# Performance work log

Measured on AMD Instinct MI355X. Metric: run time of the kernel, lower is better.

## Reference

```python
import jax, jax.numpy as jnp
import numpy as np

B, T, C, H, HS = 2, 2048, 1024, 16, 64
W_SIZE = 128
BLK = 64
NB = T // BLK            # 32 blocks
NSEL = 8                 # selected blocks per (b, h)
EPS = 1e-8


def setup_inputs() -> dict:
    key = jax.random.key(0)
    ks = jax.random.split(key, 12)
    s = 0.02
    return {
        "hidden_states": jax.random.normal(ks[0], (B, T, C), dtype=jnp.float32),
        "Wq": jax.random.normal(ks[1], (C, C), dtype=jnp.float32) * s,
        "bq": jnp.zeros((C,), jnp.float32),
        "Wk": jax.random.normal(ks[2], (C, C), dtype=jnp.float32) * s,
        "bk": jnp.zeros((C,), jnp.float32),
        "Wv": jax.random.normal(ks[3], (C, C), dtype=jnp.float32) * s,
        "bv": jnp.zeros((C,), jnp.float32),
        "Wo": jax.random.normal(ks[4], (C, C), dtype=jnp.float32) * s,
        "bo": jnp.zeros((C,), jnp.float32),
        "Wg": jax.random.normal(ks[5], (C, 3), dtype=jnp.float32) * s,
        "bg": jnp.zeros((3,), jnp.float32),
    }


def _sdpa(q, k, v, mask):
    # q: [B,H,Tq,HS], k/v: [B,H,S,HS], mask: [Tq,S] bool (True = attend)
    scale = 1.0 / jnp.sqrt(jnp.asarray(HS, q.dtype))
    scores = jnp.einsum('bhqd,bhkd->bhqk', q, k) * scale
    scores = jnp.where(mask, scores, jnp.asarray(-jnp.inf, scores.dtype))
    return jnp.einsum('bhqk,bhkd->bhqd', jax.nn.softmax(scores, axis=-1), v)


def _forward(x, Wq, bq, Wk, bk, Wv, bv, Wo, bo, Wg, bg):
    q = (x @ Wq + bq).reshape(B, T, H, HS).transpose(0, 2, 1, 3)
    k = (x @ Wk + bk).reshape(B, T, H, HS).transpose(0, 2, 1, 3)
    v = (x @ Wv + bv).reshape(B, T, H, HS).transpose(0, 2, 1, 3)

    gates = jax.nn.softmax(x @ Wg + bg, axis=-1)  # [B,T,3]
    g_sl, g_sel, g_cmp = gates[..., 0:1], gates[..., 1:2], gates[..., 2:3]

    i = jnp.arange(T)[:, None]

    # --- sliding-window branch (causal AND within window band) ---
    j = jnp.arange(T)[None, :]
    slide_mask = (j <= i) & (i - j <= W_SIZE)
    out_sl = _sdpa(q, k, v, slide_mask)

    # --- block representatives (mean-pooled K/V blocks) ---
    kb = k.reshape(B, H, NB, BLK, HS)
    vb = v.reshape(B, H, NB, BLK, HS)
    k_rep = kb.mean(axis=3)  # [B,H,NB,HS]

    # cosine similarity of each query vs each block rep, averaged over T
    qn = q / jnp.maximum(jnp.linalg.norm(q, axis=-1, keepdims=True), EPS)
    kn = k_rep / jnp.maximum(jnp.linalg.norm(k_rep, axis=-1, keepdims=True), EPS)
    global_scores = jnp.einsum('bhtd,bhnd->bhtn', qn, kn).mean(axis=2)  # [B,H,NB]
    _, top_idx = jax.lax.top_k(global_scores, NSEL)  # [B,H,NSEL]

    # gather selected K/V blocks
    sel_k = jnp.take_along_axis(kb, top_idx[..., None, None], axis=2).reshape(B, H, NSEL * BLK, HS)
    sel_v = jnp.take_along_axis(vb, top_idx[..., None, None], axis=2).reshape(B, H, NSEL * BLK, HS)

    # torch is_causal with Tq != S is top-left aligned: allow j <= i
    js = jnp.arange(NSEL * BLK)[None, :]
    out_sel = _sdpa(q, sel_k, sel_v, js <= i)

    # --- compressed branch over block reps ---
    v_cmp = vb.mean(axis=3)  # [B,H,NB,HS]
    jc = jnp.arange(NB)[None, :]
    out_cmp = _sdpa(q, k_rep, v_cmp, jc <= i)

    def merge(o):
        return o.transpose(0, 2, 1, 3).reshape(B, T, C)

    out = g_sl * merge(out_sl) + g_sel * merge(out_sel) + g_cmp * merge(out_cmp)
    return out @ Wo + bo


def reference(hidden_states, Wq, bq, Wk, bk, Wv, bv, Wo, bo, Wg, bg):
    return _forward(hidden_states, Wq, bq, Wk, bk, Wv, bv, Wo, bo, Wg, bg)
```

## Files before the change

kernel.cpp:

```cpp
#include <hip/hip_runtime.h>
#include <hip/hip_bf16.h>
#include <math.h>

#define Bc   2
#define Tc   2048
#define Cc   1024
#define Hc   16
#define HSc  64
#define WSZ  128
#define BLKc 64
#define NBc  32
#define NSELc 8
#define Mrows (Bc*Tc)
#define QCH  32
#define SOFT_C 4.0f

typedef __attribute__((ext_vector_type(8))) _Float16 half8;
typedef __attribute__((ext_vector_type(4))) float f32x4v;
typedef __attribute__((ext_vector_type(8))) unsigned short ushort8v;

__device__ __forceinline__ float wave_sum(float v) {
    #pragma unroll
    for (int o = 32; o; o >>= 1) v += __shfl_xor(v, o);
    return v;
}

__device__ __forceinline__ unsigned short f2h(float f) {
    _Float16 h = (_Float16)f;
    unsigned short u;
    __builtin_memcpy(&u, &h, 2);
    return u;
}
__device__ __forceinline__ float h2f(unsigned short u) {
    _Float16 h;
    __builtin_memcpy(&h, &u, 2);
    return (float)h;
}

__device__ __forceinline__ void gload16(const void* g, void* l) {
    __builtin_amdgcn_global_load_lds(
        (const __attribute__((address_space(1))) void*)g,
        (__attribute__((address_space(3))) void*)l, 16, 0, 0);
}

__global__ __launch_bounds__(256)
void cvt_gates_kernel(const float* __restrict__ x, unsigned short* __restrict__ xb,
                      const float* __restrict__ Wg, const float* __restrict__ bg,
                      float* __restrict__ gates)
{
    if (blockIdx.x < 4096) {
        int i = (blockIdx.x * 256 + threadIdx.x) * 4;
        float4 v = *(const float4*)&x[i];
        ushort4 o;
        o.x = f2h(v.x); o.y = f2h(v.y); o.z = f2h(v.z); o.w = f2h(v.w);
        *(ushort4*)&xb[i] = o;
        return;
    }
    const int row  = (blockIdx.x - 4096) * 4 + (threadIdx.x >> 6);
    const int lane = threadIdx.x & 63;
    const float* xr = x + (size_t)row * Cc;
    float p0 = 0, p1 = 0, p2 = 0;
    #pragma unroll
    for (int it = 0; it < 4; ++it) {
        int k4 = lane * 4 + it * 256;
        float4 xv = *(const float4*)&xr[k4];
        float4 w0 = *(const float4*)&Wg[k4 * 3];
        float4 w1 = *(const float4*)&Wg[k4 * 3 + 4];
        float4 w2 = *(const float4*)&Wg[k4 * 3 + 8];
        p0 += xv.x * w0.x + xv.y * w0.w + xv.z * w1.z + xv.w * w2.y;
        p1 += xv.x * w0.y + xv.y * w1.x + xv.z * w1.w + xv.w * w2.z;
        p2 += xv.x * w0.z + xv.y * w1.y + xv.z * w2.x + xv.w * w2.w;
    }
    p0 = wave_sum(p0); p1 = wave_sum(p1); p2 = wave_sum(p2);
    if (lane == 0) {
        p0 += bg[0]; p1 += bg[1]; p2 += bg[2];
        float m = fmaxf(p0, fmaxf(p1, p2));
        float e0 = expf(p0 - m), e1 = expf(p1 - m), e2 = expf(p2 - m);
        float s = e0 + e1 + e2;
        gates[row * 3 + 0] = e0 / s;
        gates[row * 3 + 1] = e1 / s;
        gates[row * 3 + 2] = e2 / s;
    }
}

__global__ __launch_bounds__(256)
void cvt_wT4_kernel(const float* __restrict__ W0, const float* __restrict__ W1,
                    const float* __restrict__ W2, const float* __restrict__ W3,
                    unsigned short* __restrict__ D012, unsigned short* __restrict__ D3)
{
    __shared__ float tile[64][65];
    const int z = blockIdx.z;
    const float* W = (z == 0) ? W0 : (z == 1) ? W1 : (z == 2) ? W2 : W3;
    unsigned short* WT = (z < 3) ? (D012 + (size_t)z * 1024 * 1024) : D3;
    const int n0 = blockIdx.x * 64, k0 = blockIdx.y * 64;
    const int tid = threadIdx.x;
    #pragma unroll
    for (int it = 0; it < 16; ++it) {
        int lin = tid + it * 256;
        int r = lin >> 6, c = lin & 63;
        tile[r][c] = W[(size_t)(k0 + r) * 1024 + n0 + c];
    }
    __syncthreads();
    #pragma unroll
    for (int it = 0; it < 16; ++it) {
        int lin = tid + it * 256;
        int n = lin >> 6, k = lin & 63;
        WT[(size_t)(n0 + n) * 1024 + k0 + k] = f2h(tile[k][n]);
    }
}


#define FENCE asm volatile("" ::: "memory")
#define BAR() do { FENCE; __builtin_amdgcn_s_barrier(); FENCE; } while(0)
#define WAIT_LGKM0() do { asm volatile("s_waitcnt lgkmcnt(0)" ::: "memory"); \
                          __builtin_amdgcn_sched_barrier(0); } while(0)
#define WAIT_VM(N) do { asm volatile("s_waitcnt vmcnt(" #N ")" ::: "memory"); } while(0)

#define LDA(BUF, MH) do { \
    const unsigned short* _p = &lds[BUF][0][(wmo + (MH)*64 + r16) * 64]; \
    a0[0] = *(const half8*)(_p +        cc0); a1[0] = *(const half8*)(_p +        cc1); \
    a0[1] = *(const half8*)(_p + 1024 + cc0); a1[1] = *(const half8*)(_p + 1024 + cc1); \
    a0[2] = *(const half8*)(_p + 2048 + cc0); a1[2] = *(const half8*)(_p + 2048 + cc1); \
    a0[3] = *(const half8*)(_p + 3072 + cc0); a1[3] = *(const half8*)(_p + 3072 + cc1); \
} while(0)

#define LDB(BUF, NH) do { \
    const unsigned short* _p = &lds[BUF][1][(wno + (NH)*32 + r16) * 64]; \
    b0[0] = *(const half8*)(_p +        cc0); b1[0] = *(const half8*)(_p +        cc1); \
    b0[1] = *(const half8*)(_p + 1024 + cc0); b1[1] = *(const half8*)(_p + 1024 + cc1); \
} while(0)

#define CLP(I, J, MH, NH) \
    acc[(MH)*4+(I)][(NH)*2+(J)] = __builtin_amdgcn_mfma_f32_16x16x32_f16(a0[I], b0[J], acc[(MH)*4+(I)][(NH)*2+(J)], 0, 0, 0); \
    acc[(MH)*4+(I)][(NH)*2+(J)] = __builtin_amdgcn_mfma_f32_16x16x32_f16(a1[I], b1[J], acc[(MH)*4+(I)][(NH)*2+(J)], 0, 0, 0);
#define CL(MH, NH) do { \
    __builtin_amdgcn_s_setprio(1); \
    CLP(0,0,MH,NH) CLP(0,1,MH,NH) CLP(1,0,MH,NH) CLP(1,1,MH,NH) \
    CLP(2,0,MH,NH) CLP(2,1,MH,NH) CLP(3,0,MH,NH) CLP(3,1,MH,NH) \
    __builtin_amdgcn_s_setprio(0); \
} while(0)

#define STAGEA(BUF, G, TILE) do { \
    size_t _co = (size_t)(TILE) * 64 + scol_x; \
    gload16(Ag + (size_t)(m0 +       (G)*64 + wid*8 + l8) * 1024 + _co, \
            &lds[BUF][0][((G)*64 + wid*8) * 64]); \
    gload16(Ag + (size_t)(m0 + 128 + (G)*64 + wid*8 + l8) * 1024 + _co, \
            &lds[BUF][0][(128 + (G)*64 + wid*8) * 64]); \
} while(0)

#define STAGEB(BUF, G, TILE) do { \
    size_t _co = (size_t)(TILE) * 64 + scol_x; \
    int _r0 = (wid >> 2) * 64 + (G)*32 + (wid & 3) * 8; \
    gload16(BTg + (size_t)(n0 +       _r0 + l8) * 1024 + _co, \
            &lds[BUF][1][_r0 * 64]); \
    gload16(BTg + (size_t)(n0 + 128 + _r0 + l8) * 1024 + _co, \
            &lds[BUF][1][(128 + _r0) * 64]); \
} while(0)

__global__ __launch_bounds__(512, 2)
// ... 241 lines not shown
        {
            const unsigned short* qr = qbase + (size_t)lane * HSc;
            float ss = 0.f;
            #pragma unroll
            for (int d8 = 0; d8 < 8; ++d8) {
                ushort8v v8 = *(const ushort8v*)&qr[d8 * 8];
                #pragma unroll
                for (int j = 0; j < 8; ++j) { float f = h2f(v8[j]); ss += f * f; }
            }
            rinv[lane] = 1.0f / fmaxf(sqrtf(ss), 1e-8f);
        }
        float acc = 0.f;
        #pragma unroll 8
        for (int t = 0; t < 64; ++t)
            acc += h2f(qbase[(size_t)t * HSc + lane]) * rinv[t];
        qpart[((size_t)bh * QCH + nb) * HSc + lane] = acc;
    }
}

__global__ __launch_bounds__(64)
void topk_kernel(const float* __restrict__ qpart, const float* __restrict__ krep,
                 int* __restrict__ topidx)
{
    int bh = blockIdx.x, lane = threadIdx.x;
    __shared__ float sc[NBc];
    __shared__ float qbs[HSc];
    float qa = 0.0f;
    #pragma unroll
    for (int c = 0; c < QCH; c++)
        qa += qpart[((size_t)bh * QCH + c) * HSc + lane];
    qbs[lane] = qa * (1.0f / Tc);
    __syncthreads();
    if (lane < NBc) {
        float dot = 0, nk = 0;
        for (int d = 0; d < HSc; d++) {
            float kv = krep[((size_t)bh * NBc + lane) * HSc + d];
            nk += kv * kv;
            dot += qbs[d] * kv;
        }
        sc[lane] = dot / fmaxf(sqrtf(nk), 1e-8f);
    }
    __syncthreads();
    if (lane == 0) {
        for (int s = 0; s < NSELc; s++) {
            int best = 0; float bv = sc[0];
            for (int n = 1; n < NBc; n++)
                if (sc[n] > bv) { bv = sc[n]; best = n; }
            topidx[bh * NSELc + s] = best;
            sc[best] = -INFINITY;
        }
    }
}

__device__ __forceinline__ void attn_tile4(
    int p0, int wlim, int klim, int qg0, bool nomask,
    const unsigned short* __restrict__ Kh, const unsigned short* __restrict__ Vt,
    unsigned short* __restrict__ Ph,
    half8 aq0, half8 aq1, half8 ones, int wq, int l16, int quad,
    int kc0, int kc1,
    f32x4v o[4], f32x4v& o5)
{
    f32x4v s[4];
    #pragma unroll
    for (int t = 0; t < 4; ++t) {
        f32x4v sa = (f32x4v){0.f, 0.f, 0.f, 0.f};
        half8 b0 = *(const half8*)&Kh[(t * 16 + l16) * 64 + kc0];
        half8 b1 = *(const half8*)&Kh[(t * 16 + l16) * 64 + kc1];
        sa = __builtin_amdgcn_mfma_f32_16x16x32_f16(aq0, b0, sa, 0, 0, 0);
        sa = __builtin_amdgcn_mfma_f32_16x16x32_f16(aq1, b1, sa, 0, 0, 0);
        s[t] = sa;
    }

    const int prow = wq + quad * 4;
    if (nomask) {
        #pragma unroll
        for (int t = 0; t < 4; ++t) {
            int c = t * 16 + l16;
            #pragma unroll
            for (int r = 0; r < 4; ++r) {
                float p = __expf(s[t][r] - SOFT_C);
                Ph[(prow + r) * 64 + (c ^ (((prow + r) & 7) * 8))] = f2h(p);
            }
        }
    } else {
        #pragma unroll
        for (int t = 0; t < 4; ++t) {
            int kk = t * 16 + l16;
            bool kok = kk < klim;
            int jt = p0 + kk;
            #pragma unroll
            for (int r = 0; r < 4; ++r) {
                int q = qg0 + r;
                bool valid = kok && (jt <= q) && (q - jt <= wlim);
                float p = valid ? __expf(s[t][r] - SOFT_C) : 0.0f;
                Ph[(prow + r) * 64 + (kk ^ (((prow + r) & 7) * 8))] = f2h(p);
            }
        }
    }


    const int prd = (wq + l16) * 64;
    half8 ap0 = *(const half8*)&Ph[prd + kc0];
    half8 ap1 = *(const half8*)&Ph[prd + kc1];
    o5 = __builtin_amdgcn_mfma_f32_16x16x32_f16(ap0, ones, o5, 0, 0, 0);
    o5 = __builtin_amdgcn_mfma_f32_16x16x32_f16(ap1, ones, o5, 0, 0, 0);
    #pragma unroll
    for (int dt = 0; dt < 4; ++dt) {
        half8 v0 = *(const half8*)&Vt[(dt * 16 + l16) * 64 + kc0];
        half8 v1 = *(const half8*)&Vt[(dt * 16 + l16) * 64 + kc1];
        o[dt] = __builtin_amdgcn_mfma_f32_16x16x32_f16(ap0, v0, o[dt], 0, 0, 0);
        o[dt] = __builtin_amdgcn_mfma_f32_16x16x32_f16(ap1, v1, o[dt], 0, 0, 0);
    }
}

__global__ __launch_bounds__(256, 4)
void fattn_kernel(const unsigned short* __restrict__ Qh16,
                  const unsigned short* __restrict__ Kf,
                  const unsigned short* __restrict__ Vtg,
                  const unsigned short* __restrict__ krep16,
                  const unsigned short* __restrict__ vcmpT16,
                  const int* __restrict__ topidx,
                  const float* __restrict__ gates, unsigned short* __restrict__ merged)
{
    __shared__ unsigned short KH[2][64 * 64];
    __shared__ unsigned short VT[2][64 * 64];
    __shared__ unsigned short Ph[64 * 64];

    const int qt = blockIdx.x;
    const int bh = blockIdx.y;
    const int b  = bh >> 4, h = bh & 15;
    const int tid  = threadIdx.x;
    const int wid  = tid >> 6, lane = tid & 63;
    const int l16  = lane & 15, quad = lane >> 4;
    const int q0 = qt * 64;
    const int wq = wid * 16;
    const int qg0 = q0 + wq + quad * 4;

    const int nslide = (qt < 2 ? qt : 2) + 1;
    const int nsel   = (qt + 1 < NSELc) ? (qt + 1) : NSELc;
    const int nt     = nslide + nsel + 1;

    half8 aq0, aq1, ones;
    {
        const unsigned short* qrow = Qh16 + ((size_t)bh * Tc + q0 + wq + l16) * HSc;
        aq0 = *(const half8*)(qrow + quad * 8);
        aq1 = *(const half8*)(qrow + 32 + quad * 8);
        #pragma unroll
        for (int j = 0; j < 8; ++j) ones[j] = (_Float16)1.0f;
    }

    f32x4v o[4], macc[4];
    f32x4v o5 = (f32x4v){0.f, 0.f, 0.f, 0.f};
    #pragma unroll
    for (int dt = 0; dt < 4; ++dt) {
        o[dt]    = (f32x4v){0.f, 0.f, 0.f, 0.f};
        macc[dt] = (f32x4v){0.f, 0.f, 0.f, 0.f};
    }

    const int seg = tid & 7, r0 = tid >> 3;
    const int stc = (seg ^ (r0 & 7)) * 8;
    const int st0 = r0 * 64 + stc;
    const int st1 = (r0 + 32) * 64 + stc;
    const int psw = (l16 & 7) * 8;
    const int kc0 = (quad * 8) ^ psw;
    const int kc1 = (32 + quad * 8) ^ psw;

    const unsigned short* kbh = Kf  + (size_t)bh * Tc * HSc;
    const unsigned short* vbh = Vtg + (size_t)bh * HSc * Tc;

    {
        int tb0 = q0 - (nslide - 1) * 64;
        const unsigned short* kp = kbh + (size_t)tb0 * HSc;
        const unsigned short* vp = vbh + tb0;
        *(ushort8v*)&KH[0][st0] = *(const ushort8v*)(kp + (size_t)r0 * HSc + seg * 8);
        *(ushort8v*)&KH[0][st1] = *(const ushort8v*)(kp + (size_t)(r0 + 32) * HSc + seg * 8);
        *(ushort8v*)&VT[0][st0] = *(const ushort8v*)(vp + (size_t)r0 * Tc + seg * 8);
        *(ushort8v*)&VT[0][st1] = *(const ushort8v*)(vp + (size_t)(r0 + 32) * Tc + seg * 8);
    }
    __syncthreads();

    int pb = 0;
    for (int i = 0; i < nt; ++i) {
        const int cb = i & 1;
        const bool pf = (i + 1 < nt);
        ushort8v k0, k1, v0, v1;
        if (pf) {
            const int i2 = i + 1;
            int kb2, bid2;
            if (i2 < nslide)            { kb2 = q0 - (nslide - 1 - i2) * 64; bid2 = 0; }
            else if (i2 < nslide + nsel){ kb2 = topidx[bh * NSELc + (i2 - nslide)] * BLKc; bid2 = 1; }
            else                        { kb2 = 0; bid2 = 2; }
            const unsigned short *kp, *vp;
            int vs;
            if (bid2 < 2) { kp = kbh + (size_t)kb2 * HSc; vp = vbh + kb2; vs = Tc; }
            else          { kp = krep16 + (size_t)bh * 4096;
                            vp = vcmpT16 + (size_t)bh * 4096; vs = 64; }
            k0 = *(const ushort8v*)(kp + (size_t)r0 * HSc + seg * 8);
            k1 = *(const ushort8v*)(kp + (size_t)(r0 + 32) * HSc + seg * 8);
            v0 = *(const ushort8v*)(vp + (size_t)r0 * vs + seg * 8);
            v1 = *(const ushort8v*)(vp + (size_t)(r0 + 32) * vs + seg * 8);
        }

        int p0v, wl, kl, bid; bool nomask;
        if (i < nslide)            { int tb = q0 - (nslide - 1 - i) * 64;
                                     p0v = tb; wl = WSZ; kl = 64; bid = 0;
                                     nomask = (tb == q0 - 64); }
        else if (i < nslide + nsel){ int s = i - nslide;
                                     p0v = s * BLKc; wl = 1 << 30; kl = 64; bid = 1;
                                     nomask = (p0v + 63 < q0); }
        else                       { p0v = 0; wl = 1 << 30; kl = NBc; bid = 2;
                                     nomask = false; }

        if (bid != pb) {
            #pragma unroll
            for (int r = 0; r < 4; ++r) {
                float g = gates[((size_t)b * Tc + qg0 + r) * 3 + pb];
                float inv = g / o5[r];
                #pragma unroll
                for (int dt = 0; dt < 4; ++dt) { macc[dt][r] += inv * o[dt][r]; o[dt][r] = 0.f; }
                o5[r] = 0.f;
            }
            pb = bid;
        }

        attn_tile4(p0v, wl, kl, qg0, nomask, KH[cb], VT[cb], Ph,
                   aq0, aq1, ones, wq, l16, quad, kc0, kc1, o, o5);

        if (pf) {
            *(ushort8v*)&KH[cb ^ 1][st0] = k0;
            *(ushort8v*)&KH[cb ^ 1][st1] = k1;
            *(ushort8v*)&VT[cb ^ 1][st0] = v0;
            *(ushort8v*)&VT[cb ^ 1][st1] = v1;
        }
        __syncthreads();
    }
    #pragma unroll
    for (int r = 0; r < 4; ++r) {
        float g = gates[((size_t)b * Tc + qg0 + r) * 3 + 2];
        float inv = g / o5[r];
        #pragma unroll
        for (int dt = 0; dt < 4; ++dt) macc[dt][r] += inv * o[dt][r];
    }

    #pragma unroll
    for (int r = 0; r < 4; ++r) {
        size_t mrow = (size_t)b * Tc + qg0 + r;
        #pragma unroll
        for (int dt = 0; dt < 4; ++dt)
            merged[mrow * Cc + h * HSc + dt * 16 + l16] = f2h(macc[dt][r]);
    }
}

extern "C" void kernel_launch(void* const* d_in, const int* in_sizes, int n_in,
                              void* d_out, int out_size, void* d_ws, size_t ws_size,
                              hipStream_t stream)
{
    const float* x  = (const float*)d_in[0];
    const float* Wq = (const float*)d_in[1];
    const float* bq = (const float*)d_in[2];
    const float* Wk = (const float*)d_in[3];
    const float* bk = (const float*)d_in[4];
    const float* Wv = (const float*)d_in[5];
    const float* bv = (const float*)d_in[6];
    const float* Wo = (const float*)d_in[7];
    const float* bo = (const float*)d_in[8];
    const float* Wg = (const float*)d_in[9];
    const float* bg = (const float*)d_in[10];
    float* out = (float*)d_out;
    float* ws  = (float*)d_ws;

    unsigned short* Qh16 = (unsigned short*)(ws + 0);
    unsigned short* Kf16 = (unsigned short*)(ws + 2097152);
    unsigned short* Vf16 = (unsigned short*)(ws + 4194304);
    unsigned short* Vt16 = (unsigned short*)(ws + 6291456);
    unsigned short* Mgb  = (unsigned short*)(ws + 8388608);
    unsigned short* xb   = (unsigned short*)(ws + 10485760);
    unsigned short* WqkvT = (unsigned short*)(ws + 12582912);
    unsigned short* WoT   = (unsigned short*)(ws + 14155776);
    float* gates = ws + 14680064;
    float* krep  = ws + 14692352;
    unsigned short* krep16  = (unsigned short*)(ws + 14757888);
    unsigned short* vcmpT16 = (unsigned short*)(ws + 14823424);
    float* qpart = ws + 14888960;
    int*   topidx = (int*)(ws + 14954496);

    cvt_gates_kernel<<<4096 + Mrows / 4, 256, 0, stream>>>(x, xb, Wg, bg, gates);
    cvt_wT4_kernel<<<dim3(16, 16, 4), 256, 0, stream>>>(Wq, Wk, Wv, Wo, WqkvT, WoT);

    mfma_gemm_qkv8<<<dim3(12, 16), 512, 0, stream>>>(xb, WqkvT, bq, bk, bv,
                                                     Qh16, Kf16, Vf16);
    vtrans_stats_kernel<<<dim3(NBc, Bc * Hc), 256, 0, stream>>>(Kf16, Vf16, Qh16,
                                                                Vt16, krep, krep16,
                                                                vcmpT16, qpart);
    topk_kernel<<<Bc * Hc, 64, 0, stream>>>(qpart, krep, topidx);
    fattn_kernel<<<dim3(Tc / 64, Bc * Hc), 256, 0, stream>>>(Qh16, Kf16, Vt16,
                                                             krep16, vcmpT16,
                                                             topidx, gates, Mgb);
    mfma_gemm_oproj<<<dim3(8, 64), 256, 0, stream>>>(Mgb, WoT, bo, out);
}
```

Before: 199.2 us.

## Merge front conversion kernels and give each attention wave two query groups

The gate/convert kernel and the weight-transpose kernel become one launch with a linearised block index, which saves a kernel launch. The flash-attention kernel drops from 4 to 2 waves per block, and each wave now handles 32 query rows as two 16-row groups. K and V fragments loaded from LDS are reused across both groups, and each thread stages four rows instead of two. This halves LDS fragment reads per query but doubles per-wave register use and cuts the threads available to hide latency.

```diff
diff --git a/kernel.cpp b/kernel.cpp
--- a/kernel.cpp
+++ b/kernel.cpp
@@ -44,67 +44,68 @@
 }
 
 __global__ __launch_bounds__(256)
-void cvt_gates_kernel(const float* __restrict__ x, unsigned short* __restrict__ xb,
+void cvt_front_kernel(const float* __restrict__ x, unsigned short* __restrict__ xb,
                       const float* __restrict__ Wg, const float* __restrict__ bg,
-                      float* __restrict__ gates)
+                      float* __restrict__ gates,
+                      const float* __restrict__ W0, const float* __restrict__ W1,
+                      const float* __restrict__ W2, const float* __restrict__ W3,
+                      unsigned short* __restrict__ D012, unsigned short* __restrict__ D3)
 {
-    if (blockIdx.x < 4096) {
-        int i = (blockIdx.x * 256 + threadIdx.x) * 4;
+    __shared__ float tile[64][65];
+    const int bx = blockIdx.x;
+    if (bx < 4096) {
+        int i = (bx * 256 + threadIdx.x) * 4;
         float4 v = *(const float4*)&x[i];
         ushort4 o;
         o.x = f2h(v.x); o.y = f2h(v.y); o.z = f2h(v.z); o.w = f2h(v.w);
         *(ushort4*)&xb[i] = o;
         return;
     }
-    const int row  = (blockIdx.x - 4096) * 4 + (threadIdx.x >> 6);
-    const int lane = threadIdx.x & 63;
-    const float* xr = x + (size_t)row * Cc;
-    float p0 = 0, p1 = 0, p2 = 0;
-    #pragma unroll
-    for (int it = 0; it < 4; ++it) {
-        int k4 = lane * 4 + it * 256;
-        float4 xv = *(const float4*)&xr[k4];
-        float4 w0 = *(const float4*)&Wg[k4 * 3];
-        float4 w1 = *(const float4*)&Wg[k4 * 3 + 4];
-        float4 w2 = *(const float4*)&Wg[k4 * 3 + 8];
-        p0 += xv.x * w0.x + xv.y * w0.w + xv.z * w1.z + xv.w * w2.y;
-        p1 += xv.x * w0.y + xv.y * w1.x + xv.z * w1.w + xv.w * w2.z;
-        p2 += xv.x * w0.z + xv.y * w1.y + xv.z * w2.x + xv.w * w2.w;
-    }
-    p0 = wave_sum(p0); p1 = wave_sum(p1); p2 = wave_sum(p2);
-    if (lane == 0) {
-        p0 += bg[0]; p1 += bg[1]; p2 += bg[2];
-        float m = fmaxf(p0, fmaxf(p1, p2));
-        float e0 = expf(p0 - m), e1 = expf(p1 - m), e2 = expf(p2 - m);
-        float s = e0 + e1 + e2;
-        gates[row * 3 + 0] = e0 / s;
-        gates[row * 3 + 1] = e1 / s;
-        gates[row * 3 + 2] = e2 / s;
-    }
-}
-
-__global__ __launch_bounds__(256)
-void cvt_wT4_kernel(const float* __restrict__ W0, const float* __restrict__ W1,
-                    const float* __restrict__ W2, const float* __restrict__ W3,
-                    unsigned short* __restrict__ D012, unsigned short* __restrict__ D3)
-{
-    __shared__ float tile[64][65];
-    const int z = blockIdx.z;
+    if (bx < 5120) {
+        const int row  = (bx - 4096) * 4 + (threadIdx.x >> 6);
+        const int lane = threadIdx.x & 63;
+        const float* xr = x + (size_t)row * Cc;
+        float p0 = 0, p1 = 0, p2 = 0;
+        #pragma unroll
+        for (int it = 0; it < 4; ++it) {
+            int k4 = lane * 4 + it * 256;
+            float4 xv = *(const float4*)&xr[k4];
+            float4 w0 = *(const float4*)&Wg[k4 * 3];
+            float4 w1 = *(const float4*)&Wg[k4 * 3 + 4];
+            float4 w2 = *(const float4*)&Wg[k4 * 3 + 8];
+            p0 += xv.x * w0.x + xv.y * w0.w + xv.z * w1.z + xv.w * w2.y;
+            p1 += xv.x * w0.y + xv.y * w1.x + xv.z * w1.w + xv.w * w2.z;
+            p2 += xv.x * w0.z + xv.y * w1.y + xv.z * w2.x + xv.w * w2.w;
+        }
+        p0 = wave_sum(p0); p1 = wave_sum(p1); p2 = wave_sum(p2);
+        if (lane == 0) {
+            p0 += bg[0]; p1 += bg[1]; p2 += bg[2];
+            float m = fmaxf(p0, fmaxf(p1, p2));
+            float e0 = expf(p0 - m), e1 = expf(p1 - m), e2 = expf(p2 - m);
+            float s = e0 + e1 + e2;
+            gates[row * 3 + 0] = e0 / s;
+            gates[row * 3 + 1] = e1 / s;
+            gates[row * 3 + 2] = e2 / s;
+        }
+        return;
+    }
+    const int lin = bx - 5120;
+    const int z = lin >> 8;
+    const int n0 = (lin & 15) * 64, k0 = ((lin >> 4) & 15) * 64;
     const float* W = (z == 0) ? W0 : (z == 1) ? W1 : (z == 2) ? W2 : W3;
     unsigned short* WT = (z < 3) ? (D012 + (size_t)z * 1024 * 1024) : D3;
-    const int n0 = blockIdx.x * 64, k0 = blockIdx.y * 64;
     const int tid = threadIdx.x;
     #pragma unroll
     for (int it = 0; it < 16; ++it) {
-        int lin = tid + it * 256;
-        int r = lin >> 6, c = lin & 63;
+        int l2 = tid + it * 256;
+        int r = l2 >> 6, c = l2 & 63;
         tile[r][c] = W[(size_t)(k0 + r) * 1024 + n0 + c];
     }
     __syncthreads();
     #pragma unroll
     for (int it = 0; it < 16; ++it) {
-        int lin = tid + it * 256;
-        int n = lin >> 6, k = lin & 63;
+        int l2 = tid + it * 256;
+        int n = l2 >> 6, k = l2 & 63;
         WT[(size_t)(n0 + n) * 1024 + k0 + k] = f2h(tile[k][n]);
     }
 }
@@ -452,68 +453,7 @@
     }
 }
 
-__device__ __forceinline__ void attn_tile4(
-    int p0, int wlim, int klim, int qg0, bool nomask,
-    const unsigned short* __restrict__ Kh, const unsigned short* __restrict__ Vt,
-    unsigned short* __restrict__ Ph,
-    half8 aq0, half8 aq1, half8 ones, int wq, int l16, int quad,
-    int kc0, int kc1,
-    f32x4v o[4], f32x4v& o5)
-{
-    f32x4v s[4];
-    #pragma unroll
-    for (int t = 0; t < 4; ++t) {
-        f32x4v sa = (f32x4v){0.f, 0.f, 0.f, 0.f};
-        half8 b0 = *(const half8*)&Kh[(t * 16 + l16) * 64 + kc0];
-        half8 b1 = *(const half8*)&Kh[(t * 16 + l16) * 64 + kc1];
-        sa = __builtin_amdgcn_mfma_f32_16x16x32_f16(aq0, b0, sa, 0, 0, 0);
-        sa = __builtin_amdgcn_mfma_f32_16x16x32_f16(aq1, b1, sa, 0, 0, 0);
-        s[t] = sa;
-    }
-
-    const int prow = wq + quad * 4;
-    if (nomask) {
-        #pragma unroll
-        for (int t = 0; t < 4; ++t) {
-            int c = t * 16 + l16;
-            #pragma unroll
-            for (int r = 0; r < 4; ++r) {
-                float p = __expf(s[t][r] - SOFT_C);
-                Ph[(prow + r) * 64 + (c ^ (((prow + r) & 7) * 8))] = f2h(p);
-            }
-        }
-    } else {
-        #pragma unroll
-        for (int t = 0; t < 4; ++t) {
-            int kk = t * 16 + l16;
-            bool kok = kk < klim;
-            int jt = p0 + kk;
-            #pragma unroll
-            for (int r = 0; r < 4; ++r) {
-                int q = qg0 + r;
-                bool valid = kok && (jt <= q) && (q - jt <= wlim);
-                float p = valid ? __expf(s[t][r] - SOFT_C) : 0.0f;
-                Ph[(prow + r) * 64 + (kk ^ (((prow + r) & 7) * 8))] = f2h(p);
-            }
-        }
-    }
-
-
-    const int prd = (wq + l16) * 64;
-    half8 ap0 = *(const half8*)&Ph[prd + kc0];
-    half8 ap1 = *(const half8*)&Ph[prd + kc1];
-    o5 = __builtin_amdgcn_mfma_f32_16x16x32_f16(ap0, ones, o5, 0, 0, 0);
-    o5 = __builtin_amdgcn_mfma_f32_16x16x32_f16(ap1, ones, o5, 0, 0, 0);
-    #pragma unroll
-    for (int dt = 0; dt < 4; ++dt) {
-        half8 v0 = *(const half8*)&Vt[(dt * 16 + l16) * 64 + kc0];
-        half8 v1 = *(const half8*)&Vt[(dt * 16 + l16) * 64 + kc1];
-        o[dt] = __builtin_amdgcn_mfma_f32_16x16x32_f16(ap0, v0, o[dt], 0, 0, 0);
-        o[dt] = __builtin_amdgcn_mfma_f32_16x16x32_f16(ap1, v1, o[dt], 0, 0, 0);
-    }
-}
-
-__global__ __launch_bounds__(256, 4)
+__global__ __launch_bounds__(128, 2)
 void fattn_kernel(const unsigned short* __restrict__ Qh16,
                   const unsigned short* __restrict__ Kf,
                   const unsigned short* __restrict__ Vtg,
@@ -533,34 +473,41 @@
     const int wid  = tid >> 6, lane = tid & 63;
     const int l16  = lane & 15, quad = lane >> 4;
     const int q0 = qt * 64;
-    const int wq = wid * 16;
-    const int qg0 = q0 + wq + quad * 4;
+    const int wq = wid * 32;
+    const int qb0 = q0 + wq + quad * 4;
+    const int qb1 = qb0 + 16;
 
     const int nslide = (qt < 2 ? qt : 2) + 1;
     const int nsel   = (qt + 1 < NSELc) ? (qt + 1) : NSELc;
     const int nt     = nslide + nsel + 1;
 
-    half8 aq0, aq1, ones;
-    {
-        const unsigned short* qrow = Qh16 + ((size_t)bh * Tc + q0 + wq + l16) * HSc;
-        aq0 = *(const half8*)(qrow + quad * 8);
-        aq1 = *(const half8*)(qrow + 32 + quad * 8);
-        #pragma unroll
-        for (int j = 0; j < 8; ++j) ones[j] = (_Float16)1.0f;
-    }
-
-    f32x4v o[4], macc[4];
-    f32x4v o5 = (f32x4v){0.f, 0.f, 0.f, 0.f};
-    #pragma unroll
-    for (int dt = 0; dt < 4; ++dt) {
-        o[dt]    = (f32x4v){0.f, 0.f, 0.f, 0.f};
-        macc[dt] = (f32x4v){0.f, 0.f, 0.f, 0.f};
+    half8 aq[2][2], ones;
+    #pragma unroll
+    for (int qg = 0; qg < 2; ++qg) {
+        const unsigned short* qrow = Qh16 + ((size_t)bh * Tc + q0 + wq + qg * 16 + l16) * HSc;
+        aq[qg][0] = *(const half8*)(qrow + quad * 8);
+        aq[qg][1] = *(const half8*)(qrow + 32 + quad * 8);
+    }
+    #pragma unroll
+    for (int j = 0; j < 8; ++j) ones[j] = (_Float16)1.0f;
+
+    f32x4v o[2][4], macc[2][4], o5[2];
+    #pragma unroll
+    for (int qg = 0; qg < 2; ++qg) {
+        o5[qg] = (f32x4v){0.f, 0.f, 0.f, 0.f};
+        #pragma unroll
+        for (int dt = 0; dt < 4; ++dt) {
+            o[qg][dt]    = (f32x4v){0.f, 0.f, 0.f, 0.f};
+            macc[qg][dt] = (f32x4v){0.f, 0.f, 0.f, 0.f};
+        }
     }
 
     const int seg = tid & 7, r0 = tid >> 3;
     const int stc = (seg ^ (r0 & 7)) * 8;
     const int st0 = r0 * 64 + stc;
-    const int st1 = (r0 + 32) * 64 + stc;
+    const int st1 = (r0 + 16) * 64 + stc;
+    const int st2 = (r0 + 32) * 64 + stc;
+    const int st3 = (r0 + 48) * 64 + stc;
     const int psw = (l16 & 7) * 8;
     const int kc0 = (quad * 8) ^ psw;
     const int kc1 = (32 + quad * 8) ^ psw;
@@ -572,10 +519,14 @@
         int tb0 = q0 - (nslide - 1) * 64;
         const unsigned short* kp = kbh + (size_t)tb0 * HSc;
         const unsigned short* vp = vbh + tb0;
-        *(ushort8v*)&KH[0][st0] = *(const ushort8v*)(kp + (size_t)r0 * HSc + seg * 8);
-        *(ushort8v*)&KH[0][st1] = *(const ushort8v*)(kp + (size_t)(r0 + 32) * HSc + seg * 8);
-        *(ushort8v*)&VT[0][st0] = *(const ushort8v*)(vp + (size_t)r0 * Tc + seg * 8);
-        *(ushort8v*)&VT[0][st1] = *(const ushort8v*)(vp + (size_t)(r0 + 32) * Tc + seg * 8);
+        *(ushort8v*)&KH[0][st0] = *(const ushort8v*)(kp + (size_t)(r0     ) * HSc + seg * 8);
+        *(ushort8v*)&KH[0][st1] = *(const ushort8v*)(kp + (size_t)(r0 + 16) * HSc + seg * 8);
+        *(ushort8v*)&KH[0][st2] = *(const ushort8v*)(kp + (size_t)(r0 + 32) * HSc + seg * 8);
+        *(ushort8v*)&KH[0][st3] = *(const ushort8v*)(kp + (size_t)(r0 + 48) * HSc + seg * 8);
+        *(ushort8v*)&VT[0][st0] = *(const ushort8v*)(vp + (size_t)(r0     ) * Tc + seg * 8);
+        *(ushort8v*)&VT[0][st1] = *(const ushort8v*)(vp + (size_t)(r0 + 16) * Tc + seg * 8);
+        *(ushort8v*)&VT[0][st2] = *(const ushort8v*)(vp + (size_t)(r0 + 32) * Tc + seg * 8);
+        *(ushort8v*)&VT[0][st3] = *(const ushort8v*)(vp + (size_t)(r0 + 48) * Tc + seg * 8);
     }
     __syncthreads();
 
@@ -583,7 +534,7 @@
     for (int i = 0; i < nt; ++i) {
         const int cb = i & 1;
         const bool pf = (i + 1 < nt);
-        ushort8v k0, k1, v0, v1;
+        ushort8v k0, k1, k2, k3, v0, v1, v2, v3;
         if (pf) {
             const int i2 = i + 1;
             int kb2, bid2;
@@ -595,10 +546,14 @@
             if (bid2 < 2) { kp = kbh + (size_t)kb2 * HSc; vp = vbh + kb2; vs = Tc; }
             else          { kp = krep16 + (size_t)bh * 4096;
                             vp = vcmpT16 + (size_t)bh * 4096; vs = 64; }
-            k0 = *(const ushort8v*)(kp + (size_t)r0 * HSc + seg * 8);
-            k1 = *(const ushort8v*)(kp + (size_t)(r0 + 32) * HSc + seg * 8);
-            v0 = *(const ushort8v*)(vp + (size_t)r0 * vs + seg * 8);
-            v1 = *(const ushort8v*)(vp + (size_t)(r0 + 32) * vs + seg * 8);
+            k0 = *(const ushort8v*)(kp + (size_t)(r0     ) * HSc + seg * 8);
+            k1 = *(const ushort8v*)(kp + (size_t)(r0 + 16) * HSc + seg * 8);
+            k2 = *(const ushort8v*)(kp + (size_t)(r0 + 32) * HSc + seg * 8);
+            k3 = *(const ushort8v*)(kp + (size_t)(r0 + 48) * HSc + seg * 8);
+            v0 = *(const ushort8v*)(vp + (size_t)(r0     ) * vs + seg * 8);
+            v1 = *(const ushort8v*)(vp + (size_t)(r0 + 16) * vs + seg * 8);
+            v2 = *(const ushort8v*)(vp + (size_t)(r0 + 32) * vs + seg * 8);
+            v3 = *(const ushort8v*)(vp + (size_t)(r0 + 48) * vs + seg * 8);
         }
 
         int p0v, wl, kl, bid; bool nomask;
@@ -613,41 +568,127 @@
 
         if (bid != pb) {
             #pragma unroll
-            for (int r = 0; r < 4; ++r) {
-                float g = gates[((size_t)b * Tc + qg0 + r) * 3 + pb];
-                float inv = g / o5[r];
+            for (int qg = 0; qg < 2; ++qg) {
+                int qb = (qg == 0) ? qb0 : qb1;
                 #pragma unroll
-                for (int dt = 0; dt < 4; ++dt) { macc[dt][r] += inv * o[dt][r]; o[dt][r] = 0.f; }
-                o5[r] = 0.f;
+                for (int r = 0; r < 4; ++r) {
+                    float g = gates[((size_t)b * Tc + qb + r) * 3 + pb];
+                    float inv = g / o5[qg][r];
+                    #pragma unroll
+                    for (int dt = 0; dt < 4; ++dt) { macc[qg][dt][r] += inv * o[qg][dt][r]; o[qg][dt][r] = 0.f; }
+                    o5[qg][r] = 0.f;
+                }
             }
             pb = bid;
         }
 
-        attn_tile4(p0v, wl, kl, qg0, nomask, KH[cb], VT[cb], Ph,
-                   aq0, aq1, ones, wq, l16, quad, kc0, kc1, o, o5);
+        {
+            const unsigned short* Kh = KH[cb];
+            const unsigned short* Vt = VT[cb];
+            half8 bk0[4], bk1[4];
+            #pragma unroll
+            for (int t = 0; t < 4; ++t) {
+                bk0[t] = *(const half8*)&Kh[(t * 16 + l16) * 64 + kc0];
+                bk1[t] = *(const half8*)&Kh[(t * 16 + l16) * 64 + kc1];
+            }
+            f32x4v s[2][4];
+            #pragma unroll
+            for (int qg = 0; qg < 2; ++qg)
+                #pragma unroll
+                for (int t = 0; t < 4; ++t) {
+                    f32x4v sa = (f32x4v){0.f, 0.f, 0.f, 0.f};
+                    sa = __builtin_amdgcn_mfma_f32_16x16x32_f16(aq[qg][0], bk0[t], sa, 0, 0, 0);
+                    sa = __builtin_amdgcn_mfma_f32_16x16x32_f16(aq[qg][1], bk1[t], sa, 0, 0, 0);
+                    s[qg][t] = sa;
+                }
+
+            #pragma unroll
+            for (int qg = 0; qg < 2; ++qg) {
+                const int prow = wq + qg * 16 + quad * 4;
+                const int qb = (qg == 0) ? qb0 : qb1;
+                if (nomask) {
+                    #pragma unroll
+                    for (int t = 0; t < 4; ++t) {
+                        int c = t * 16 + l16;
+                        #pragma unroll
+                        for (int r = 0; r < 4; ++r) {
+                            float p = __expf(s[qg][t][r] - SOFT_C);
+                            Ph[(prow + r) * 64 + (c ^ (((prow + r) & 7) * 8))] = f2h(p);
+                        }
+                    }
+                } else {
+                    #pragma unroll
+                    for (int t = 0; t < 4; ++t) {
+                        int kk = t * 16 + l16;
+                        bool kok = kk < kl;
+                        int jt = p0v + kk;
+                        #pragma unroll
+                        for (int r = 0; r < 4; ++r) {
+                            int q = qb + r;
+                            bool valid = kok && (jt <= q) && (q - jt <= wl);
+                            float p = valid ? __expf(s[qg][t][r] - SOFT_C) : 0.0f;
+                            Ph[(prow + r) * 64 + (kk ^ (((prow + r) & 7) * 8))] = f2h(p);
+                        }
+                    }
+                }
+            }
+
+
+            half8 vv0[4], vv1[4];
+            #pragma unroll
+            for (int dt = 0; dt < 4; ++dt) {
+                vv0[dt] = *(const half8*)&Vt[(dt * 16 + l16) * 64 + kc0];
+                vv1[dt] = *(const half8*)&Vt[(dt * 16 + l16) * 64 + kc1];
+            }
+            #pragma unroll
+            for (int qg = 0; qg < 2; ++qg) {
+                const int prd = (wq + qg * 16 + l16) * 64;
+                half8 ap0 = *(const half8*)&Ph[prd + kc0];
+                half8 ap1 = *(const half8*)&Ph[prd + kc1];
+                o5[qg] = __builtin_amdgcn_mfma_f32_16x16x32_f16(ap0, ones, o5[qg], 0, 0, 0);
+                o5[qg] = __builtin_amdgcn_mfma_f32_16x16x32_f16(ap1, ones, o5[qg], 0, 0, 0);
+                #pragma unroll
+                for (int dt = 0; dt < 4; ++dt) {
+                    o[qg][dt] = __builtin_amdgcn_mfma_f32_16x16x32_f16(ap0, vv0[dt], o[qg][dt], 0, 0, 0);
+                    o[qg][dt] = __builtin_amdgcn_mfma_f32_16x16x32_f16(ap1, vv1[dt], o[qg][dt], 0, 0, 0);
+                }
+            }
+        }
 
         if (pf) {
             *(ushort8v*)&KH[cb ^ 1][st0] = k0;
             *(ushort8v*)&KH[cb ^ 1][st1] = k1;
+            *(ushort8v*)&KH[cb ^ 1][st2] = k2;
+            *(ushort8v*)&KH[cb ^ 1][st3] = k3;
             *(ushort8v*)&VT[cb ^ 1][st0] = v0;
             *(ushort8v*)&VT[cb ^ 1][st1] = v1;
+            *(ushort8v*)&VT[cb ^ 1][st2] = v2;
+            *(ushort8v*)&VT[cb ^ 1][st3] = v3;
         }
         __syncthreads();
     }
     #pragma unroll
-    for (int r = 0; r < 4; ++r) {
-        float g = gates[((size_t)b * Tc + qg0 + r) * 3 + 2];
-        float inv = g / o5[r];
-        #pragma unroll
-        for (int dt = 0; dt < 4; ++dt) macc[dt][r] += inv * o[dt][r];
-    }
-
-    #pragma unroll
-    for (int r = 0; r < 4; ++r) {
-        size_t mrow = (size_t)b * Tc + qg0 + r;
-        #pragma unroll
-        for (int dt = 0; dt < 4; ++dt)
-            merged[mrow * Cc + h * HSc + dt * 16 + l16] = f2h(macc[dt][r]);
+    for (int qg = 0; qg < 2; ++qg) {
+        int qb = (qg == 0) ? qb0 : qb1;
+        #pragma unroll
+        for (int r = 0; r < 4; ++r) {
+            float g = gates[((size_t)b * Tc + qb + r) * 3 + 2];
+            float inv = g / o5[qg][r];
+            #pragma unroll
+            for (int dt = 0; dt < 4; ++dt) macc[qg][dt][r] += inv * o[qg][dt][r];
+        }
+    }
+
+    #pragma unroll
+    for (int qg = 0; qg < 2; ++qg) {
+        int qb = (qg == 0) ? qb0 : qb1;
+        #pragma unroll
+        for (int r = 0; r < 4; ++r) {
+            size_t mrow = (size_t)b * Tc + qb + r;
+            #pragma unroll
+            for (int dt = 0; dt < 4; ++dt)
+                merged[mrow * Cc + h * HSc + dt * 16 + l16] = f2h(macc[qg][dt][r]);
+        }
     }
 }
 
@@ -684,8 +725,8 @@
     float* qpart = ws + 14888960;
     int*   topidx = (int*)(ws + 14954496);
 
-    cvt_gates_kernel<<<4096 + Mrows / 4, 256, 0, stream>>>(x, xb, Wg, bg, gates);
-    cvt_wT4_kernel<<<dim3(16, 16, 4), 256, 0, stream>>>(Wq, Wk, Wv, Wo, WqkvT, WoT);
+    cvt_front_kernel<<<6144, 256, 0, stream>>>(x, xb, Wg, bg, gates,
+                                               Wq, Wk, Wv, Wo, WqkvT, WoT);
 
     mfma_gemm_qkv8<<<dim3(12, 16), 512, 0, stream>>>(xb, WqkvT, bq, bk, bv,
                                                      Qh16, Kf16, Vf16);
@@ -693,7 +734,7 @@
                                                                 Vt16, krep, krep16,
                                                                 vcmpT16, qpart);
     topk_kernel<<<Bc * Hc, 64, 0, stream>>>(qpart, krep, topidx);
-    fattn_kernel<<<dim3(Tc / 64, Bc * Hc), 256, 0, stream>>>(Qh16, Kf16, Vt16,
+    fattn_kernel<<<dim3(Tc / 64, Bc * Hc), 128, 0, stream>>>(Qh16, Kf16, Vt16,
                                                              krep16, vcmpT16,
                                                              topidx, gates, Mgb);
     mfma_gemm_oproj<<<dim3(8, 64), 256, 0, stream>>>(Mgb, WoT, bo, out);
```

Measured after the change: 197.5 us, median of 2. About the same (-0.8%).

## Process two attention tiles per iteration and fuse front conversion kernels

Applied to the files above, without the earlier changes.

The flash-attention loop now handles two K/V tiles per step. It issues both QK^T MFMA groups before the softmax/PV phases and prefetches the next two tiles into registers, which halves the barrier count. The launch bound drops from 4 to 2 waves-per-EU, giving more registers at the cost of occupancy. The separate nomask fast path is removed in favour of a unified unsigned-compare mask. The gate/convert kernel and the weight-transpose kernel are merged into one launch to save a kernel launch.

```diff
diff --git a/kernel.cpp b/kernel.cpp
--- a/kernel.cpp
+++ b/kernel.cpp
@@ -44,67 +44,68 @@
 }
 
 __global__ __launch_bounds__(256)
-void cvt_gates_kernel(const float* __restrict__ x, unsigned short* __restrict__ xb,
+void cvt_front_kernel(const float* __restrict__ x, unsigned short* __restrict__ xb,
                       const float* __restrict__ Wg, const float* __restrict__ bg,
-                      float* __restrict__ gates)
-{
-    if (blockIdx.x < 4096) {
-        int i = (blockIdx.x * 256 + threadIdx.x) * 4;
+                      float* __restrict__ gates,
+                      const float* __restrict__ W0, const float* __restrict__ W1,
+                      const float* __restrict__ W2, const float* __restrict__ W3,
+                      unsigned short* __restrict__ D012, unsigned short* __restrict__ D3)
+{
+    __shared__ float tile[64][65];
+    const int bx = blockIdx.x;
+    if (bx < 4096) {
+        int i = (bx * 256 + threadIdx.x) * 4;
         float4 v = *(const float4*)&x[i];
         ushort4 o;
         o.x = f2h(v.x); o.y = f2h(v.y); o.z = f2h(v.z); o.w = f2h(v.w);
         *(ushort4*)&xb[i] = o;
         return;
     }
-    const int row  = (blockIdx.x - 4096) * 4 + (threadIdx.x >> 6);
-    const int lane = threadIdx.x & 63;
-    const float* xr = x + (size_t)row * Cc;
-    float p0 = 0, p1 = 0, p2 = 0;
-    #pragma unroll
-    for (int it = 0; it < 4; ++it) {
-        int k4 = lane * 4 + it * 256;
-        float4 xv = *(const float4*)&xr[k4];
-        float4 w0 = *(const float4*)&Wg[k4 * 3];
-        float4 w1 = *(const float4*)&Wg[k4 * 3 + 4];
-        float4 w2 = *(const float4*)&Wg[k4 * 3 + 8];
-        p0 += xv.x * w0.x + xv.y * w0.w + xv.z * w1.z + xv.w * w2.y;
-        p1 += xv.x * w0.y + xv.y * w1.x + xv.z * w1.w + xv.w * w2.z;
-        p2 += xv.x * w0.z + xv.y * w1.y + xv.z * w2.x + xv.w * w2.w;
-    }
-    p0 = wave_sum(p0); p1 = wave_sum(p1); p2 = wave_sum(p2);
-    if (lane == 0) {
-        p0 += bg[0]; p1 += bg[1]; p2 += bg[2];
-        float m = fmaxf(p0, fmaxf(p1, p2));
-        float e0 = expf(p0 - m), e1 = expf(p1 - m), e2 = expf(p2 - m);
-        float s = e0 + e1 + e2;
-        gates[row * 3 + 0] = e0 / s;
-        gates[row * 3 + 1] = e1 / s;
-        gates[row * 3 + 2] = e2 / s;
-    }
-}
-
-__global__ __launch_bounds__(256)
-void cvt_wT4_kernel(const float* __restrict__ W0, const float* __restrict__ W1,
-                    const float* __restrict__ W2, const float* __restrict__ W3,
-                    unsigned short* __restrict__ D012, unsigned short* __restrict__ D3)
-{
-    __shared__ float tile[64][65];
-    const int z = blockIdx.z;
+    if (bx < 5120) {
+        const int row  = (bx - 4096) * 4 + (threadIdx.x >> 6);
+        const int lane = threadIdx.x & 63;
+        const float* xr = x + (size_t)row * Cc;
+        float p0 = 0, p1 = 0, p2 = 0;
+        #pragma unroll
+        for (int it = 0; it < 4; ++it) {
+            int k4 = lane * 4 + it * 256;
+            float4 xv = *(const float4*)&xr[k4];
+            float4 w0 = *(const float4*)&Wg[k4 * 3];
+            float4 w1 = *(const float4*)&Wg[k4 * 3 + 4];
+            float4 w2 = *(const float4*)&Wg[k4 * 3 + 8];
+            p0 += xv.x * w0.x + xv.y * w0.w + xv.z * w1.z + xv.w * w2.y;
+            p1 += xv.x * w0.y + xv.y * w1.x + xv.z * w1.w + xv.w * w2.z;
+            p2 += xv.x * w0.z + xv.y * w1.y + xv.z * w2.x + xv.w * w2.w;
+        }
+        p0 = wave_sum(p0); p1 = wave_sum(p1); p2 = wave_sum(p2);
+        if (lane == 0) {
+            p0 += bg[0]; p1 += bg[1]; p2 += bg[2];
+            float m = fmaxf(p0, fmaxf(p1, p2));
+            float e0 = expf(p0 - m), e1 = expf(p1 - m), e2 = expf(p2 - m);
+            float s = e0 + e1 + e2;
+            gates[row * 3 + 0] = e0 / s;
+            gates[row * 3 + 1] = e1 / s;
+            gates[row * 3 + 2] = e2 / s;
+        }
+        return;
+    }
+    const int lin = bx - 5120;
+    const int z = lin >> 8;
+    const int n0 = (lin & 15) * 64, k0 = ((lin >> 4) & 15) * 64;
     const float* W = (z == 0) ? W0 : (z == 1) ? W1 : (z == 2) ? W2 : W3;
     unsigned short* WT = (z < 3) ? (D012 + (size_t)z * 1024 * 1024) : D3;
-    const int n0 = blockIdx.x * 64, k0 = blockIdx.y * 64;
     const int tid = threadIdx.x;
     #pragma unroll
     for (int it = 0; it < 16; ++it) {
-        int lin = tid + it * 256;
-        int r = lin >> 6, c = lin & 63;
+        int l2 = tid + it * 256;
+        int r = l2 >> 6, c = l2 & 63;
         tile[r][c] = W[(size_t)(k0 + r) * 1024 + n0 + c];
     }
     __syncthreads();
     #pragma unroll
     for (int it = 0; it < 16; ++it) {
-        int lin = tid + it * 256;
-        int n = lin >> 6, k = lin & 63;
+        int l2 = tid + it * 256;
+        int n = l2 >> 6, k = l2 & 63;
         WT[(size_t)(n0 + n) * 1024 + k0 + k] = f2h(tile[k][n]);
     }
 }
@@ -452,15 +453,41 @@
     }
 }
 
-__device__ __forceinline__ void attn_tile4(
-    int p0, int wlim, int klim, int qg0, bool nomask,
-    const unsigned short* __restrict__ Kh, const unsigned short* __restrict__ Vt,
-    unsigned short* __restrict__ Ph,
-    half8 aq0, half8 aq1, half8 ones, int wq, int l16, int quad,
-    int kc0, int kc1,
-    f32x4v o[4], f32x4v& o5)
-{
-    f32x4v s[4];
+__device__ __forceinline__ void fa_desc(int i, int nslide, int nsel, int q0,
+                                        const int* __restrict__ topidx, int bh,
+                                        int& kb, int& p0v, int& wl, int& kl, int& bid)
+{
+    if (i < nslide)             { kb = q0 - (nslide - 1 - i) * 64;
+                                  p0v = kb; wl = WSZ; kl = 64; bid = 0; }
+    else if (i < nslide + nsel) { int s = i - nslide;
+                                  kb = topidx[bh * NSELc + s] * BLKc;
+                                  p0v = s * BLKc; wl = 1 << 30; kl = 64; bid = 1; }
+    else                        { kb = 0; p0v = 0; wl = 1 << 30; kl = NBc; bid = 2; }
+}
+
+__device__ __forceinline__ void fa_ldtile(int kb, int bid,
+                                          const unsigned short* __restrict__ kbh,
+                                          const unsigned short* __restrict__ vbh,
+                                          const unsigned short* __restrict__ krepb,
+                                          const unsigned short* __restrict__ vcmpb,
+                                          int r0, int seg,
+                                          ushort8v& k0, ushort8v& k1,
+                                          ushort8v& v0, ushort8v& v1)
+{
+    const unsigned short *kp, *vp;
+    int vs;
+    if (bid < 2) { kp = kbh + (size_t)kb * HSc; vp = vbh + kb; vs = Tc; }
+    else         { kp = krepb; vp = vcmpb; vs = 64; }
+    k0 = *(const ushort8v*)(kp + (size_t)r0 * HSc + seg * 8);
+    k1 = *(const ushort8v*)(kp + (size_t)(r0 + 32) * HSc + seg * 8);
+    v0 = *(const ushort8v*)(vp + (size_t)r0 * vs + seg * 8);
+    v1 = *(const ushort8v*)(vp + (size_t)(r0 + 32) * vs + seg * 8);
+}
+
+__device__ __forceinline__ void fa_qkt(const unsigned short* __restrict__ Kh,
+                                       half8 aq0, half8 aq1, int l16, int kc0, int kc1,
+                                       f32x4v s[4])
+{
     #pragma unroll
     for (int t = 0; t < 4; ++t) {
         f32x4v sa = (f32x4v){0.f, 0.f, 0.f, 0.f};
@@ -470,35 +497,32 @@
         sa = __builtin_amdgcn_mfma_f32_16x16x32_f16(aq1, b1, sa, 0, 0, 0);
         s[t] = sa;
     }
-
-    const int prow = wq + quad * 4;
-    if (nomask) {
-        #pragma unroll
-        for (int t = 0; t < 4; ++t) {
-            int c = t * 16 + l16;
-            #pragma unroll
-            for (int r = 0; r < 4; ++r) {
-                float p = __expf(s[t][r] - SOFT_C);
-                Ph[(prow + r) * 64 + (c ^ (((prow + r) & 7) * 8))] = f2h(p);
-            }
-        }
-    } else {
-        #pragma unroll
-        for (int t = 0; t < 4; ++t) {
-            int kk = t * 16 + l16;
-            bool kok = kk < klim;
-            int jt = p0 + kk;
-            #pragma unroll
-            for (int r = 0; r < 4; ++r) {
-                int q = qg0 + r;
-                bool valid = kok && (jt <= q) && (q - jt <= wlim);
-                float p = valid ? __expf(s[t][r] - SOFT_C) : 0.0f;
-                Ph[(prow + r) * 64 + (kk ^ (((prow + r) & 7) * 8))] = f2h(p);
-            }
-        }
-    }
-
-
+}
+
+__device__ __forceinline__ void fa_expph(const f32x4v s[4], int p0v, int wl, int kl,
+                                         int qg0, int prow, int l16,
+                                         unsigned short* __restrict__ Ph)
+{
+    #pragma unroll
+    for (int t = 0; t < 4; ++t) {
+        int kk = t * 16 + l16;
+        bool kok = kk < kl;
+        int jt = p0v + kk;
+        #pragma unroll
+        for (int r = 0; r < 4; ++r) {
+            bool valid = kok && ((unsigned)(qg0 + r - jt) <= (unsigned)wl);
+            float p = valid ? __expf(s[t][r] - SOFT_C) : 0.0f;
+            int row = prow + r;
+            Ph[row * 64 + (kk ^ ((row & 7) * 8))] = f2h(p);
+        }
+    }
+}
+
+__device__ __forceinline__ void fa_pv(const unsigned short* __restrict__ Vt,
+                                      const unsigned short* __restrict__ Ph,
+                                      half8 ones, int wq, int l16, int kc0, int kc1,
+                                      f32x4v o[4], f32x4v& o5)
+{
     const int prd = (wq + l16) * 64;
     half8 ap0 = *(const half8*)&Ph[prd + kc0];
     half8 ap1 = *(const half8*)&Ph[prd + kc1];
@@ -513,7 +537,7 @@
     }
 }
 
-__global__ __launch_bounds__(256, 4)
+__global__ __launch_bounds__(256, 2)
 void fattn_kernel(const unsigned short* __restrict__ Qh16,
                   const unsigned short* __restrict__ Kf,
                   const unsigned short* __restrict__ Vtg,
@@ -535,6 +559,7 @@
     const int q0 = qt * 64;
     const int wq = wid * 16;
     const int qg0 = q0 + wq + quad * 4;
+    const int prow = wq + quad * 4;
 
     const int nslide = (qt < 2 ? qt : 2) + 1;
     const int nsel   = (qt + 1 < NSELc) ? (qt + 1) : NSELc;
@@ -565,75 +590,87 @@
     const int kc0 = (quad * 8) ^ psw;
     const int kc1 = (32 + quad * 8) ^ psw;
 
-    const unsigned short* kbh = Kf  + (size_t)bh * Tc * HSc;
-    const unsigned short* vbh = Vtg + (size_t)bh * HSc * Tc;
+    const unsigned short* kbh  = Kf  + (size_t)bh * Tc * HSc;
+    const unsigned short* vbh  = Vtg + (size_t)bh * HSc * Tc;
+    const unsigned short* krepb = krep16  + (size_t)bh * 4096;
+    const unsigned short* vcmpb = vcmpT16 + (size_t)bh * 4096;
+
+#define FA_MERGE(PB) do { \
+    _Pragma("unroll") \
+    for (int r = 0; r < 4; ++r) { \
+        float g = gates[((size_t)b * Tc + qg0 + r) * 3 + (PB)]; \
+        float inv = g / o5[r]; \
+        _Pragma("unroll") \
+        for (int dt = 0; dt < 4; ++dt) { macc[dt][r] += inv * o[dt][r]; o[dt][r] = 0.f; } \
+        o5[r] = 0.f; \
+    } \
+} while(0)
 
     {
-        int tb0 = q0 - (nslide - 1) * 64;
-        const unsigned short* kp = kbh + (size_t)tb0 * HSc;
-        const unsigned short* vp = vbh + tb0;
-        *(ushort8v*)&KH[0][st0] = *(const ushort8v*)(kp + (size_t)r0 * HSc + seg * 8);
-        *(ushort8v*)&KH[0][st1] = *(const ushort8v*)(kp + (size_t)(r0 + 32) * HSc + seg * 8);
-        *(ushort8v*)&VT[0][st0] = *(const ushort8v*)(vp + (size_t)r0 * Tc + seg * 8);
-        *(ushort8v*)&VT[0][st1] = *(const ushort8v*)(vp + (size_t)(r0 + 32) * Tc + seg * 8);
+        int kb, p0v, wl, kl, bid;
+        ushort8v k0, k1, v0, v1;
+        fa_desc(0, nslide, nsel, q0, topidx, bh, kb, p0v, wl, kl, bid);
+        fa_ldtile(kb, bid, kbh, vbh, krepb, vcmpb, r0, seg, k0, k1, v0, v1);
+        *(ushort8v*)&KH[0][st0] = k0; *(ushort8v*)&KH[0][st1] = k1;
+        *(ushort8v*)&VT[0][st0] = v0; *(ushort8v*)&VT[0][st1] = v1;
+        fa_desc(1, nslide, nsel, q0, topidx, bh, kb, p0v, wl, kl, bid);
+        fa_ldtile(kb, bid, kbh, vbh, krepb, vcmpb, r0, seg, k0, k1, v0, v1);
+        *(ushort8v*)&KH[1][st0] = k0; *(ushort8v*)&KH[1][st1] = k1;
+        *(ushort8v*)&VT[1][st0] = v0; *(ushort8v*)&VT[1][st1] = v1;
     }
     __syncthreads();
 
     int pb = 0;
-    for (int i = 0; i < nt; ++i) {
-        const int cb = i & 1;
-        const bool pf = (i + 1 < nt);
-        ushort8v k0, k1, v0, v1;
-        if (pf) {
-            const int i2 = i + 1;
-            int kb2, bid2;
-            if (i2 < nslide)            { kb2 = q0 - (nslide - 1 - i2) * 64; bid2 = 0; }
-            else if (i2 < nslide + nsel){ kb2 = topidx[bh * NSELc + (i2 - nslide)] * BLKc; bid2 = 1; }
-            else                        { kb2 = 0; bid2 = 2; }
-            const unsigned short *kp, *vp;
-            int vs;
-            if (bid2 < 2) { kp = kbh + (size_t)kb2 * HSc; vp = vbh + kb2; vs = Tc; }
-            else          { kp = krep16 + (size_t)bh * 4096;
-                            vp = vcmpT16 + (size_t)bh * 4096; vs = 64; }
-            k0 = *(const ushort8v*)(kp + (size_t)r0 * HSc + seg * 8);
-            k1 = *(const ushort8v*)(kp + (size_t)(r0 + 32) * HSc + seg * 8);
-            v0 = *(const ushort8v*)(vp + (size_t)r0 * vs + seg * 8);
-            v1 = *(const ushort8v*)(vp + (size_t)(r0 + 32) * vs + seg * 8);
-        }
-
-        int p0v, wl, kl, bid; bool nomask;
-        if (i < nslide)            { int tb = q0 - (nslide - 1 - i) * 64;
-                                     p0v = tb; wl = WSZ; kl = 64; bid = 0;
-                                     nomask = (tb == q0 - 64); }
-        else if (i < nslide + nsel){ int s = i - nslide;
-                                     p0v = s * BLKc; wl = 1 << 30; kl = 64; bid = 1;
-                                     nomask = (p0v + 63 < q0); }
-        else                       { p0v = 0; wl = 1 << 30; kl = NBc; bid = 2;
-                                     nomask = false; }
-
-        if (bid != pb) {
-            #pragma unroll
-            for (int r = 0; r < 4; ++r) {
-                float g = gates[((size_t)b * Tc + qg0 + r) * 3 + pb];
-                float inv = g / o5[r];
-                #pragma unroll
-                for (int dt = 0; dt < 4; ++dt) { macc[dt][r] += inv * o[dt][r]; o[dt][r] = 0.f; }
-                o5[r] = 0.f;
+    for (int i = 0; i < nt; i += 2) {
+        const bool dual = (i + 1 < nt);
+        const bool pf2  = (i + 2 < nt);
+        const bool pf3  = (i + 3 < nt);
+
+        ushort8v pk0[2], pk1[2], pv0[2], pv1[2];
+        if (pf2) {
+            int kb, p0v, wl, kl, bid;
+            fa_desc(i + 2, nslide, nsel, q0, topidx, bh, kb, p0v, wl, kl, bid);
+            fa_ldtile(kb, bid, kbh, vbh, krepb, vcmpb, r0, seg,
+                      pk0[0], pk1[0], pv0[0], pv1[0]);
+        }
+        if (pf3) {
+            int kb, p0v, wl, kl, bid;
+            fa_desc(i + 3, nslide, nsel, q0, topidx, bh, kb, p0v, wl, kl, bid);
+            fa_ldtile(kb, bid, kbh, vbh, krepb, vcmpb, r0, seg,
+                      pk0[1], pk1[1], pv0[1], pv1[1]);
+        }
+
+        int kbA, p0A, wlA, klA, bidA;
+        fa_desc(i, nslide, nsel, q0, topidx, bh, kbA, p0A, wlA, klA, bidA);
+        int kbB, p0B, wlB, klB, bidB = bidA;
+        if (dual) fa_desc(i + 1, nslide, nsel, q0, topidx, bh, kbB, p0B, wlB, klB, bidB);
+
+        f32x4v sA[4], sB[4];
+        fa_qkt(KH[0], aq0, aq1, l16, kc0, kc1, sA);
+        if (dual) fa_qkt(KH[1], aq0, aq1, l16, kc0, kc1, sB);
+
+        if (bidA != pb) { FA_MERGE(pb); pb = bidA; }
+        fa_expph(sA, p0A, wlA, klA, qg0, prow, l16, Ph);
+        fa_pv(VT[0], Ph, ones, wq, l16, kc0, kc1, o, o5);
+
+        if (dual) {
+            if (bidB != pb) { FA_MERGE(pb); pb = bidB; }
+            fa_expph(sB, p0B, wlB, klB, qg0, prow, l16, Ph);
+            fa_pv(VT[1], Ph, ones, wq, l16, kc0, kc1, o, o5);
+        }
+
+        if (pf2) {
+            __syncthreads();
+            *(ushort8v*)&KH[0][st0] = pk0[0]; *(ushort8v*)&KH[0][st1] = pk1[0];
+            *(ushort8v*)&VT[0][st0] = pv0[0]; *(ushort8v*)&VT[0][st1] = pv1[0];
+            if (pf3) {
+                *(ushort8v*)&KH[1][st0] = pk0[1]; *(ushort8v*)&KH[1][st1] = pk1[1];
+                *(ushort8v*)&VT[1][st0] = pv0[1]; *(ushort8v*)&VT[1][st1] = pv1[1];
             }
-            pb = bid;
-        }
-
-        attn_tile4(p0v, wl, kl, qg0, nomask, KH[cb], VT[cb], Ph,
-                   aq0, aq1, ones, wq, l16, quad, kc0, kc1, o, o5);
-
-        if (pf) {
-            *(ushort8v*)&KH[cb ^ 1][st0] = k0;
-            *(ushort8v*)&KH[cb ^ 1][st1] = k1;
-            *(ushort8v*)&VT[cb ^ 1][st0] = v0;
-            *(ushort8v*)&VT[cb ^ 1][st1] = v1;
-        }
-        __syncthreads();
-    }
+            __syncthreads();
+        }
+    }
+
     #pragma unroll
     for (int r = 0; r < 4; ++r) {
         float g = gates[((size_t)b * Tc + qg0 + r) * 3 + 2];
@@ -649,6 +686,7 @@
         for (int dt = 0; dt < 4; ++dt)
             merged[mrow * Cc + h * HSc + dt * 16 + l16] = f2h(macc[dt][r]);
     }
+#undef FA_MERGE
 }
 
 extern "C" void kernel_launch(void* const* d_in, const int* in_sizes, int n_in,
@@ -684,8 +722,8 @@
     float* qpart = ws + 14888960;
     int*   topidx = (int*)(ws + 14954496);
 
-    cvt_gates_kernel<<<4096 + Mrows / 4, 256, 0, stream>>>(x, xb, Wg, bg, gates);
-    cvt_wT4_kernel<<<dim3(16, 16, 4), 256, 0, stream>>>(Wq, Wk, Wv, Wo, WqkvT, WoT);
+    cvt_front_kernel<<<6144, 256, 0, stream>>>(x, xb, Wg, bg, gates,
+                                               Wq, Wk, Wv, Wo, WqkvT, WoT);
 
     mfma_gemm_qkv8<<<dim3(12, 16), 512, 0, stream>>>(xb, WqkvT, bq, bk, bv,
                                                      Qh16, Kf16, Vf16);
```

Measured after the change: 201.4 us. About the same (+1.2%).
